# Performance work log

Hardware: AMD Instinct MI355X
Metric: run time of the kernel (lower is better)

## Reference

```python
import jax, jax.numpy as jnp
import numpy as np

B, N_LR, N_HR, D, NH, L, K = 16, 256, 512, 512, 8, 4, 4
FF = 4 * D

def _ln(x, g, b):
    m = jnp.mean(x, -1, keepdims=True)
    v = jnp.var(x, -1, keepdims=True)
    return (x - m) * jax.lax.rsqrt(v + 1e-5) * g + b

def _gelu(x):
    return jax.nn.gelu(x, approximate=False)  # torch nn.GELU default = exact

def _attn(x, qkvW, qkvb, projW, projb, bias):
    b, n, d = x.shape
    hd = d // NH
    qkv = (x @ qkvW + qkvb).reshape(b, n, 3, NH, hd).transpose(2, 0, 3, 1, 4)
    q, k, v = qkv[0], qkv[1], qkv[2]
    a = jnp.einsum('bhnd,bhmd->bhnm', q, k) * (hd ** -0.5)
    if bias is not None:
        a = a + bias
    a = jax.nn.softmax(a, axis=-1)
    o = jnp.einsum('bhnm,bhmd->bhnd', a, v).transpose(0, 2, 1, 3).reshape(b, n, d)
    return o @ projW + projb

def _ffn(x, W1, b1, W2, b2):
    return _gelu(x @ W1 + b1) @ W2 + b2

def setup_inputs() -> dict:
    key = jax.random.key(0)
    ks = iter(jax.random.split(key, 64))
    def rn(shape, s=0.02):
        return jax.random.normal(next(ks), shape, jnp.float32) * s
    inp = {}
    A = rn((B, N_LR, N_LR), 1.0)
    A = 0.5 * (A + A.transpose(0, 2, 1))  # symmetric weighted adjacency
    inp['A_lr'] = A
    inp['X_lr'] = A  # node features = adjacency rows, as in the original model
    inp['ip_W'] = rn((N_LR, D)); inp['ip_b'] = jnp.zeros(D)
    inp['ip_g'] = jnp.ones(D); inp['ip_bt'] = jnp.zeros(D)
    inp['e_n1g'] = jnp.ones((L, D)); inp['e_n1b'] = jnp.zeros((L, D))
    inp['e_qkvW'] = rn((L, D, 3 * D)); inp['e_qkvb'] = jnp.zeros((L, 3 * D))
    inp['e_projW'] = rn((L, D, D)); inp['e_projb'] = jnp.zeros((L, D))
    inp['e_ebW'] = rn((L, NH), 1.0); inp['e_ebs'] = jnp.full((L,), 0.1)
    inp['e_n2g'] = jnp.ones((L, D)); inp['e_n2b'] = jnp.zeros((L, D))
    inp['e_f1W'] = rn((L, D, FF)); inp['e_f1b'] = jnp.zeros((L, FF))
    inp['e_f2W'] = rn((L, FF, D)); inp['e_f2b'] = jnp.zeros((L, D))
    inp['encn_g'] = jnp.ones(D); inp['encn_b'] = jnp.zeros(D)
    inp['up1W'] = rn((N_LR, N_HR)); inp['up1b'] = jnp.zeros(N_HR)
    inp['up2W'] = rn((N_HR, N_HR)); inp['up2b'] = jnp.zeros(N_HR)
    inp['r_n1g'] = jnp.ones(D); inp['r_n1b'] = jnp.zeros(D)
    inp['r_qkvW'] = rn((D, 3 * D)); inp['r_qkvb'] = jnp.zeros(3 * D)
    inp['r_projW'] = rn((D, D)); inp['r_projb'] = jnp.zeros(D)
    inp['r_n2g'] = jnp.ones(D); inp['r_n2b'] = jnp.zeros(D)
    inp['r_f1W'] = rn((D, FF)); inp['r_f1b'] = jnp.zeros(FF)
    inp['r_f2W'] = rn((FF, D)); inp['r_f2b'] = jnp.zeros(D)
    inp['hrn_g'] = jnp.ones(D); inp['hrn_b'] = jnp.zeros(D)
    inp['dec_W'] = rn((K, D, D)); inp['dec_b'] = jnp.full((1,), 3.0)
    return inp

def reference(A_lr, X_lr, ip_W, ip_b, ip_g, ip_bt, e_n1g, e_n1b, e_qkvW, e_qkvb, e_projW, e_projb, e_ebW, e_ebs, e_n2g, e_n2b, e_f1W, e_f1b, e_f2W, e_f2b, encn_g, encn_b, up1W, up1b, up2W, up2b, r_n1g, r_n1b, r_qkvW, r_qkvb, r_projW, r_projb, r_n2g, r_n2b, r_f1W, r_f1b, r_f2W, r_f2b, hrn_g, hrn_b, dec_W, dec_b):
    # input_proj: Linear -> LayerNorm -> GELU (dropout is identity in eval)
    H = _gelu(_ln(X_lr @ ip_W + ip_b, ip_g, ip_bt))  # (B, n_lr, D)
    # encoder: pre-norm blocks with additive per-head edge bias in softmax
    for l in range(L):
        bias = e_ebs[l] * A_lr[:, None, :, :] * e_ebW[l][None, :, None, None]  # (B,NH,N,N)
        H = H + _attn(_ln(H, e_n1g[l], e_n1b[l]), e_qkvW[l], e_qkvb[l], e_projW[l], e_projb[l], bias)
        H = H + _ffn(_ln(H, e_n2g[l], e_n2b[l]), e_f1W[l], e_f1b[l], e_f2W[l], e_f2b[l])
    H = _ln(H, encn_g, encn_b)
    # upsample n_lr -> n_hr along node axis (applied on transposed H)
    Ht = H.transpose(0, 2, 1)                      # (B, D, n_lr)
    Ht = _gelu(Ht @ up1W + up1b) @ up2W + up2b     # (B, D, n_hr)
    H = Ht.transpose(0, 2, 1)                      # (B, n_hr, D)
    # HR refinement: standard pre-norm self-attention block
    H = H + _attn(_ln(H, r_n1g, r_n1b), r_qkvW, r_qkvb, r_projW, r_projb, None)
    H = H + _ffn(_ln(H, r_n2g, r_n2b), r_f1W, r_f1b, r_f2W, r_f2b)
    H = _ln(H, hrn_g, hrn_b)
    # bilinear multi-head decoder: mean_k H W_k H^T, symmetrized
    A_pred = jnp.einsum('bnd,kde,bme->bnm', H, dec_W, H) / K
    A_pred = 0.5 * (A_pred + A_pred.transpose(0, 2, 1))
    iu, ju = np.triu_indices(N_HR, k=1)
    pred = A_pred[:, iu, ju]                        # (B, n_hr*(n_hr-1)/2)
    return jax.nn.softplus(pred + dec_b[0])
```

## Files before the change

kernel.cpp:

```cpp
#include <hip/hip_runtime.h>
#include <hip/hip_bf16.h>
#include <math.h>

#define DEV __device__ __forceinline__

typedef __attribute__((ext_vector_type(8))) short bf16x8;
typedef __attribute__((ext_vector_type(4))) short s16x4;
typedef __attribute__((ext_vector_type(4))) float f32x4;

DEV float gelu_f(float x) {
  float u = 1.5957691f * x * (1.0f + 0.044715f * x * x);
  return x / (1.0f + __expf(-u));
}

DEV short bf16s(float x) {
  __hip_bfloat16 v = __float2bfloat16(x);
  return *reinterpret_cast<short*>(&v);
}

DEV void async16(void* lds, const void* g) {
  __builtin_amdgcn_global_load_lds(
      (const __attribute__((address_space(1))) unsigned int*)g,
      (__attribute__((address_space(3))) unsigned int*)lds, 16, 0, 0);
}

__global__ __launch_bounds__(256) void conv2_kernel(
    const float* __restrict__ X1, __hip_bfloat16* __restrict__ Y1,
    const float* __restrict__ X2, __hip_bfloat16* __restrict__ Y2, int n) {
  int i = blockIdx.x * 256 + threadIdx.x;
  if (i < n) {
    Y1[i] = __float2bfloat16(X1[i]);
    Y2[i] = __float2bfloat16(X2[i]);
  }
}

struct CvArgs {
  const float* s[11];
  __hip_bfloat16* d[11];
};

__global__ __launch_bounds__(256) void multi_tconv_kernel(CvArgs a) {
  const int Rj[11] = {256, 512, 512, 512, 2048, 256, 512, 512, 512, 512, 2048};
  const int Cj[11] = {512, 1536, 512, 2048, 512, 512, 512, 1536, 512, 2048, 512};
  const int Nj[11] = {1, 4, 4, 4, 4, 1, 1, 1, 1, 1, 1};
  __shared__ float t[32][33];
  int rem = blockIdx.x, j = 0;
  for (; j < 11; ++j) {
    int tj = (Rj[j] >> 5) * (Cj[j] >> 5) * Nj[j];
    if (rem < tj) break;
    rem -= tj;
  }
  const int R = Rj[j], C = Cj[j];
  const int perb = (R >> 5) * (C >> 5);
  const int z = rem / perb;
  const int tt = rem % perb;
  const int tc = C >> 5;
  const int r0 = (tt / tc) << 5, c0 = (tt % tc) << 5;
  const float* xb = a.s[j] + (size_t)z * R * C;
  __hip_bfloat16* yb = a.d[j] + (size_t)z * R * C;
  int tx = threadIdx.x & 31, ty = threadIdx.x >> 5;
  for (int i = ty; i < 32; i += 8) t[i][tx] = xb[(size_t)(r0 + i) * C + c0 + tx];
  __syncthreads();
  for (int i = ty; i < 32; i += 8)
    yb[(size_t)(c0 + i) * R + r0 + tx] = __float2bfloat16(t[tx][i]);
}

__global__ __launch_bounds__(256) void build_s_kernel(
    const float* __restrict__ W, __hip_bfloat16* __restrict__ S, int D, int Kk) {
  int i = blockIdx.x * 256 + threadIdx.x;
  if (i >= D * D) return;
  int d = i / D, e = i % D;
  float s = 0.f;
  for (int k = 0; k < Kk; ++k) {
    s += W[(size_t)k * D * D + i];
    s += W[(size_t)k * D * D + (size_t)e * D + d];
  }
  S[i] = __float2bfloat16(s / (2.0f * Kk));
}

template <int NJ>
__global__ __launch_bounds__(256) void mgemm_kernel(
    const __hip_bfloat16* __restrict__ A, const __hip_bfloat16* __restrict__ Bt,
    const float* __restrict__ bias, const float* __restrict__ resid,
    float* __restrict__ outf, __hip_bfloat16* __restrict__ outb,
    int M, int N, int K, int act, int mgrp) {
  __shared__ __align__(16) short As[2][128 * 64];
  __shared__ __align__(16) short Bs[2][NJ * 32 * 64];
  const int tid = threadIdx.x;
  const int lane = tid & 63, wave = tid >> 6;
  const int quad = lane >> 4, l15 = lane & 15;
  const int wr = wave >> 1, wc = wave & 1;
  const int bid = blockIdx.x;
  const int g = bid & 7, sidx = bid >> 3;
  const int mt = g * mgrp + sidx % mgrp;
  const int nt = sidx / mgrp;
  const int row0 = mt * 128, col0 = nt * (NJ * 32);
  const short* Ag = (const short*)A;
  const short* Bg = (const short*)Bt;

  auto stage = [&](int bsel, int k0) {
#pragma unroll
    for (int i = 0; i < 4; ++i) {
      int c = i * 256 + tid;
      int r = c >> 3, pp = c & 7;
      int kc = pp ^ (r & 7);
      async16(&As[bsel][c * 8], &Ag[(size_t)(row0 + r) * K + k0 + kc * 8]);
    }
#pragma unroll
    for (int i = 0; i < NJ; ++i) {
      int c = i * 256 + tid;
      int r = c >> 3, pp = c & 7;
      int kc = pp ^ (r & 7);
      async16(&Bs[bsel][c * 8], &Bg[(size_t)(col0 + r) * K + k0 + kc * 8]);
    }
  };

  f32x4 acc[4][NJ] = {};
  const int nk = K >> 6;
  stage(0, 0);
  for (int t = 0; t < nk; ++t) {
    const int cur = t & 1;
    __syncthreads();
    if (t + 1 < nk) stage(cur ^ 1, (t + 1) << 6);
#pragma unroll
    for (int kh = 0; kh < 2; ++kh) {
      const int ch = ((quad + kh * 4) ^ (l15 & 7)) * 8;
      bf16x8 af[4], bq[NJ];
#pragma unroll
      for (int mi = 0; mi < 4; ++mi)
        af[mi] = *(const bf16x8*)&As[cur][(wr * 64 + mi * 16 + l15) * 64 + ch];
#pragma unroll
      for (int ni = 0; ni < NJ; ++ni)
        bq[ni] = *(const bf16x8*)&Bs[cur][(wc * (NJ * 16) + ni * 16 + l15) * 64 + ch];
#pragma unroll
      for (int mi = 0; mi < 4; ++mi)
#pragma unroll
        for (int ni = 0; ni < NJ; ++ni)
          acc[mi][ni] = __builtin_amdgcn_mfma_f32_16x16x32_bf16(af[mi], bq[ni], acc[mi][ni], 0, 0, 0);
    }
  }

#pragma unroll
  for (int ni = 0; ni < NJ; ++ni) {
    int cc = col0 + wc * (NJ * 16) + ni * 16 + l15;
    float bb = bias ? bias[cc] : 0.f;
#pragma unroll
    for (int mi = 0; mi < 4; ++mi) {
#pragma unroll
      for (int r = 0; r < 4; ++r) {
        int rr = row0 + wr * 64 + mi * 16 + quad * 4 + r;
        size_t idx = (size_t)rr * N + cc;
        float v = acc[mi][ni][r] + bb;
        if (act) v = gelu_f(v);
        if (resid) v += resid[idx];
        if (outf) outf[idx] = v;
        if (outb) outb[idx] = __float2bfloat16(v);
      }
    }
  }
}

__global__ __launch_bounds__(256) void qkv_gemm_kernel(
    const __hip_bfloat16* __restrict__ A, const __hip_bfloat16* __restrict__ Bt,
    const float* __restrict__ bias, __hip_bfloat16* __restrict__ qkv,
    int M, int K, int nseq, int lgn, int mgrp) {
  __shared__ __align__(16) short As[2][128 * 64];
  __shared__ __align__(16) short Bs[2][128 * 64];
  const int tid = threadIdx.x;
  const int lane = tid & 63, wave = tid >> 6;
  const int quad = lane >> 4, l15 = lane & 15;
  const int wr = wave >> 1, wc = wave & 1;
  const int bid = blockIdx.x;
  const int g = bid & 7, sidx = bid >> 3;
  const int mt = g * mgrp + sidx % mgrp;
  const int nt = sidx / mgrp;
  const int row0 = mt * 128, col0 = nt * 128;
  const short* Ag = (const short*)A;
  const short* Bg = (const short*)Bt;

  auto stage = [&](int bsel, int k0) {
#pragma unroll
    for (int i = 0; i < 4; ++i) {
      int c = i * 256 + tid;
      int r = c >> 3, pp = c & 7;
      int kc = pp ^ (r & 7);
      async16(&As[bsel][c * 8], &Ag[(size_t)(row0 + r) * K + k0 + kc * 8]);
    }
#pragma unroll
    for (int i = 0; i < 4; ++i) {
      int c = i * 256 + tid;
      int r = c >> 3, pp = c & 7;
      int kc = pp ^ (r & 7);
      async16(&Bs[bsel][c * 8], &Bg[(size_t)(col0 + r) * K + k0 + kc * 8]);
    }
  };

  f32x4 acc[4][4] = {};
  const int nk = K >> 6;
  stage(0, 0);
  for (int t = 0; t < nk; ++t) {
    const int cur = t & 1;
    __syncthreads();
    if (t + 1 < nk) stage(cur ^ 1, (t + 1) << 6);
#pragma unroll
    for (int kh = 0; kh < 2; ++kh) {
      const int ch = ((quad + kh * 4) ^ (l15 & 7)) * 8;
      bf16x8 af[4], bq[4];
#pragma unroll
      for (int mi = 0; mi < 4; ++mi)
        af[mi] = *(const bf16x8*)&As[cur][(wr * 64 + mi * 16 + l15) * 64 + ch];
#pragma unroll
      for (int ni = 0; ni < 4; ++ni)
        bq[ni] = *(const bf16x8*)&Bs[cur][(wc * 64 + ni * 16 + l15) * 64 + ch];
#pragma unroll
      for (int mi = 0; mi < 4; ++mi)
#pragma unroll
        for (int ni = 0; ni < 4; ++ni)
          acc[mi][ni] = __builtin_amdgcn_mfma_f32_16x16x32_bf16(af[mi], bq[ni], acc[mi][ni], 0, 0, 0);
    }
  }

  const size_t PART = (size_t)M * 512;
#pragma unroll
  for (int ni = 0; ni < 4; ++ni) {
    int cc = col0 + wc * 64 + ni * 16 + l15;
    float bb = bias ? bias[cc] : 0.f;
    int which = cc >> 9;
    int h = (cc >> 6) & 7;
    int d = cc & 63;
#pragma unroll
    for (int mi = 0; mi < 4; ++mi) {
#pragma unroll
      for (int r = 0; r < 4; ++r) {
        int rr = row0 + wr * 64 + mi * 16 + quad * 4 + r;
        int b = rr >> lgn;
        int nn = rr & (nseq - 1);
        float v = acc[mi][ni][r] + bb;
        size_t dst;
        if (which == 2) {
          dst = 2 * PART + (((size_t)b * 8 + h) * 64 + d) * nseq + nn;
        } else {
          dst = (size_t)which * PART + (((size_t)b * 8 + h) * nseq + nn) * 64 + d;
        }
        qkv[dst] = __float2bfloat16(v);
      }
    }
  }
}

__global__ __launch_bounds__(256) void fattn_kernel(
    const __hip_bfloat16* __restrict__ Qh, const __hip_bfloat16* __restrict__ Kh,
    const __hip_bfloat16* __restrict__ Vt, __hip_bfloat16* __restrict__ O,
    const __hip_bfloat16* __restrict__ Abias, const float* __restrict__ ebW,
    const float* __restrict__ ebs, int N, int lgq) {
  __shared__ __align__(16) short Ks[2][64 * 64];
  __shared__ __align__(16) short Vs[2][64 * 64];
  __shared__ __align__(16) short Ps[4][16][72];
  const int bid = blockIdx.x;
  const int g = bid & 7, s = bid >> 3;
  const int bloc = s >> (lgq + 3);
  const int rem = s & ((8 << lgq) - 1);
  const int h = rem >> lgq;
  const int qt = rem & ((1 << lgq) - 1);
  const int b = g * 2 + bloc;
  const int tid = threadIdx.x, lane = tid & 63, wave = tid >> 6;
  const int quad = lane >> 4, l15 = lane & 15;
  const size_t hb = (size_t)b * 8 + h;
  const short* Qg = (const short*)Qh + hb * N * 64;
  const short* Kg = (const short*)Kh + hb * N * 64;
  const short* Vg = (const short*)Vt + hb * 64 * N;
  const float scale = 0.125f;
  const bool hasb = (Abias != nullptr);
  const float bscale = hasb ? ebs[0] * ebW[h] : 0.f;
  const int qrow_w = qt * 64 + wave * 16;

  auto stageKV = [&](int bsel, int k0) {
#pragma unroll
    for (int i = 0; i < 2; ++i) {
      int c = (wave * 2 + i) * 64 + lane;
      int r = c >> 3, pp = c & 7;
      int kc = pp ^ (r & 7);
      async16(&Ks[bsel][(wave * 2 + i) * 512], &Kg[(size_t)(k0 + r) * 64 + kc * 8]);
      async16(&Vs[bsel][(wave * 2 + i) * 512], &Vg[(size_t)r * N + k0 + kc * 8]);
    }
  };

  bf16x8 qf[2];
  qf[0] = *(const bf16x8*)&Qg[(size_t)(qrow_w + l15) * 64 + quad * 8];
  qf[1] = *(const bf16x8*)&Qg[(size_t)(qrow_w + l15) * 64 + quad * 8 + 32];

  float l_r[4] = {0.f, 0.f, 0.f, 0.f};
  f32x4 oacc[4] = {};

  const int ntl = N >> 6;
  stageKV(0, 0);
  for (int t = 0; t < ntl; ++t) {
    const int cur = t & 1;
    const int k0 = t << 6;
    __syncthreads();
    if (t + 1 < ntl) stageKV(cur ^ 1, (t + 1) << 6);

    f32x4 sv[4] = {};
#pragma unroll
    for (int kh = 0; kh < 2; ++kh) {
      const int ch = ((quad + kh * 4) ^ (l15 & 7)) * 8;
#pragma unroll
      for (int ni = 0; ni < 4; ++ni) {
        bf16x8 kf = *(const bf16x8*)&Ks[cur][(ni * 16 + l15) * 64 + ch];
        sv[ni] = __builtin_amdgcn_mfma_f32_16x16x32_bf16(qf[kh], kf, sv[ni], 0, 0, 0);
      }
    }
    if (hasb) {
#pragma unroll
      for (int ni = 0; ni < 4; ++ni)
#pragma unroll
        for (int r = 0; r < 4; ++r) {
          int qq = qrow_w + quad * 4 + r;
          int kk = k0 + ni * 16 + l15;
          float ab = __bfloat162float(Abias[((size_t)b * N + qq) * N + kk]);
          sv[ni][r] = sv[ni][r] * scale + bscale * ab;
        }
    } else {
#pragma unroll
      for (int ni = 0; ni < 4; ++ni)
#pragma unroll
        for (int r = 0; r < 4; ++r) sv[ni][r] *= scale;
    }

#pragma unroll
    for (int ni = 0; ni < 4; ++ni)
#pragma unroll
      for (int r = 0; r < 4; ++r) {
        float p = __expf(sv[ni][r]);
        sv[ni][r] = p;
        l_r[r] += p;
      }

#pragma unroll
    for (int ni = 0; ni < 4; ++ni)
#pragma unroll
      for (int r = 0; r < 4; ++r)
        Ps[wave][quad * 4 + r][ni * 16 + l15] = bf16s(sv[ni][r]);

    bf16x8 pf0 = *(const bf16x8*)&Ps[wave][l15][quad * 8];
    bf16x8 pf1 = *(const bf16x8*)&Ps[wave][l15][quad * 8 + 32];
#pragma unroll
    for (int kh = 0; kh < 2; ++kh) {
      const int ch = ((quad + kh * 4) ^ (l15 & 7)) * 8;
#pragma unroll
      for (int ni = 0; ni < 4; ++ni) {
        bf16x8 vf = *(const bf16x8*)&Vs[cur][(ni * 16 + l15) * 64 + ch];
        oacc[ni] = __builtin_amdgcn_mfma_f32_16x16x32_bf16(kh ? pf1 : pf0, vf, oacc[ni], 0, 0, 0);
      }
    }
  }

#pragma unroll
  for (int off = 1; off < 16; off <<= 1)
#pragma unroll
    for (int r = 0; r < 4; ++r) l_r[r] += __shfl_xor(l_r[r], off, 64);
  float inv[4];
#pragma unroll
  for (int r = 0; r < 4; ++r) inv[r] = 1.f / l_r[r];
#pragma unroll
  for (int ni = 0; ni < 4; ++ni)
#pragma unroll
    for (int r = 0; r < 4; ++r) {
      int nn = qrow_w + quad * 4 + r;
      int col = h * 64 + ni * 16 + l15;
      O[((size_t)b * N + nn) * 512 + col] = __float2bfloat16(oacc[ni][r] * inv[r]);
    }
}

__global__ __launch_bounds__(256) void dec_mfma_kernel(
    const __hip_bfloat16* __restrict__ Tb_, const __hip_bfloat16* __restrict__ Hb_,
    const float* __restrict__ dec_b, float* __restrict__ out) {
  const int Nn = 512, K = 512;
  __shared__ __align__(16) short As[2][64 * 64];
  __shared__ __align__(16) short Bs[2][64 * 64];
  int p = blockIdx.x;
  int bb = blockIdx.y;
  int it = 0, rem = p;
  while (rem >= 8 - it) { rem -= 8 - it; ++it; }
  int jt = it + rem;
  const int row0 = it * 64, col0 = jt * 64;
  const int tid = threadIdx.x;
  const int lane = tid & 63, wave = tid >> 6;
  const int quad = lane >> 4, l15 = lane & 15;
  const int wr = (wave >> 1) * 32, wc = (wave & 1) * 32;
  const short* Ag = (const short*)(Tb_ + (size_t)bb * Nn * K);
  const short* Bg = (const short*)(Hb_ + (size_t)bb * Nn * K);

  auto stage = [&](int bsel, int k0) {
#pragma unroll
    for (int i = 0; i < 2; ++i) {
      int c = (wave * 2 + i) * 64 + lane;
      int r = c >> 3, pp = c & 7;
      int kc = pp ^ (r & 7);
      async16(&As[bsel][(wave * 2 + i) * 512], &Ag[(size_t)(row0 + r) * K + k0 + kc * 8]);
      async16(&Bs[bsel][(wave * 2 + i) * 512], &Bg[(size_t)(col0 + r) * K + k0 + kc * 8]);
    }
  };

  f32x4 acc[2][2] = {};
  const int nk = K >> 6;
  stage(0, 0);
  for (int t = 0; t < nk; ++t) {
    const int cur = t & 1;
    __syncthreads();
    if (t + 1 < nk) stage(cur ^ 1, (t + 1) << 6);
#pragma unroll
    for (int kh = 0; kh < 2; ++kh) {
      const int ch = ((quad + kh * 4) ^ (l15 & 7)) * 8;
      bf16x8 af[2], bq[2];
#pragma unroll
      for (int mi = 0; mi < 2; ++mi)
        af[mi] = *(const bf16x8*)&As[cur][(wr + mi * 16 + l15) * 64 + ch];
#pragma unroll
      for (int ni = 0; ni < 2; ++ni)
        bq[ni] = *(const bf16x8*)&Bs[cur][(wc + ni * 16 + l15) * 64 + ch];
#pragma unroll
      for (int mi = 0; mi < 2; ++mi)
#pragma unroll
        for (int ni = 0; ni < 2; ++ni)
          acc[mi][ni] = __builtin_amdgcn_mfma_f32_16x16x32_bf16(af[mi], bq[ni], acc[mi][ni], 0, 0, 0);
    }
  }

  float db = dec_b[0];
  size_t obase = (size_t)bb * ((size_t)Nn * (Nn - 1) / 2);
#pragma unroll
  for (int mi = 0; mi < 2; ++mi) {
#pragma unroll
    for (int ni = 0; ni < 2; ++ni) {
      int j = col0 + wc + ni * 16 + l15;
#pragma unroll
      for (int r = 0; r < 4; ++r) {
        int i = row0 + wr + mi * 16 + quad * 4 + r;
        if (j > i) {
          float x = acc[mi][ni][r] + db;
          float sp = fmaxf(x, 0.f) + __logf(1.f + __expf(-fabsf(x)));
          out[obase + (size_t)i * (2 * Nn - i - 1) / 2 + (j - i - 1)] = sp;
        }
      }
    }
  }
}

__global__ __launch_bounds__(256) void ln_kernel(
    const float* __restrict__ X, float* __restrict__ outf,
    __hip_bfloat16* __restrict__ outb, const float* __restrict__ g,
    const float* __restrict__ b, int do_gelu) {
  const int row = blockIdx.x * 4 + (threadIdx.x >> 6);
  const int lane = threadIdx.x & 63;
  const float4* x = (const float4*)X + (size_t)row * 128;
  float4 v0 = x[lane], v1 = x[lane + 64];
  float s = v0.x + v0.y + v0.z + v0.w + v1.x + v1.y + v1.z + v1.w;
  float s2 = v0.x * v0.x + v0.y * v0.y + v0.z * v0.z + v0.w * v0.w +
             v1.x * v1.x + v1.y * v1.y + v1.z * v1.z + v1.w * v1.w;
#pragma unroll
  for (int off = 32; off; off >>= 1) {
    s += __shfl_xor(s, off, 64);
    s2 += __shfl_xor(s2, off, 64);
  }
  const float mean = s * (1.0f / 512.0f);
  const float inv = rsqrtf(s2 * (1.0f / 512.0f) - mean * mean + 1e-5f);
  const float4 g0 = ((const float4*)g)[lane], g1 = ((const float4*)g)[lane + 64];
  const float4 b0 = ((const float4*)b)[lane], b1 = ((const float4*)b)[lane + 64];
  float4 y0, y1;
  y0.x = (v0.x - mean) * inv * g0.x + b0.x;
  y0.y = (v0.y - mean) * inv * g0.y + b0.y;
  y0.z = (v0.z - mean) * inv * g0.z + b0.z;
  y0.w = (v0.w - mean) * inv * g0.w + b0.w;
  y1.x = (v1.x - mean) * inv * g1.x + b1.x;
  y1.y = (v1.y - mean) * inv * g1.y + b1.y;
  y1.z = (v1.z - mean) * inv * g1.z + b1.z;
  y1.w = (v1.w - mean) * inv * g1.w + b1.w;
  if (do_gelu) {
    y0.x = gelu_f(y0.x); y0.y = gelu_f(y0.y); y0.z = gelu_f(y0.z); y0.w = gelu_f(y0.w);
    y1.x = gelu_f(y1.x); y1.y = gelu_f(y1.y); y1.z = gelu_f(y1.z); y1.w = gelu_f(y1.w);
  }
  if (outf) {
    float4* of = (float4*)outf + (size_t)row * 128;
    of[lane] = y0;
    of[lane + 64] = y1;
  }
  if (outb) {
    s16x4 p0, p1;
    p0.x = bf16s(y0.x); p0.y = bf16s(y0.y); p0.z = bf16s(y0.z); p0.w = bf16s(y0.w);
    p1.x = bf16s(y1.x); p1.y = bf16s(y1.y); p1.z = bf16s(y1.z); p1.w = bf16s(y1.w);
    *(s16x4*)((short*)outb + (size_t)row * 512 + lane * 4) = p0;
    *(s16x4*)((short*)outb + (size_t)row * 512 + 256 + lane * 4) = p1;
  }
}

template <typename T>
__global__ __launch_bounds__(256) void transpose_kernel(
    const T* __restrict__ X, T* __restrict__ Y, int R, int C) {
  __shared__ T t[32][33];
  const T* xb = X + (size_t)blockIdx.z * R * C;
  T* yb = Y + (size_t)blockIdx.z * R * C;
  int c0 = blockIdx.x * 32, r0 = blockIdx.y * 32;
  int tx = threadIdx.x & 31, ty = threadIdx.x >> 5;
  for (int i = ty; i < 32; i += 8) t[i][tx] = xb[(size_t)(r0 + i) * C + c0 + tx];
  __syncthreads();
  for (int i = ty; i < 32; i += 8) yb[(size_t)(c0 + i) * R + r0 + tx] = t[tx][i];
}

extern "C" void kernel_launch(void* const* d_in, const int* in_sizes, int n_in,
                              void* d_out, int out_size, void* d_ws, size_t ws_size,
                              hipStream_t stream) {
  const float *A_lr = (const float*)d_in[0], *X_lr = (const float*)d_in[1],
              *ip_W = (const float*)d_in[2], *ip_b = (const float*)d_in[3],
              *ip_g = (const float*)d_in[4], *ip_bt = (const float*)d_in[5],
              *e_n1g = (const float*)d_in[6], *e_n1b = (const float*)d_in[7],
              *e_qkvW = (const float*)d_in[8], *e_qkvb = (const float*)d_in[9],
              *e_projW = (const float*)d_in[10], *e_projb = (const float*)d_in[11],
              *e_ebW = (const float*)d_in[12], *e_ebs = (const float*)d_in[13],
              *e_n2g = (const float*)d_in[14], *e_n2b = (const float*)d_in[15],
              *e_f1W = (const float*)d_in[16], *e_f1b = (const float*)d_in[17],
              *e_f2W = (const float*)d_in[18], *e_f2b = (const float*)d_in[19],
              *encn_g = (const float*)d_in[20], *encn_b = (const float*)d_in[21],
              *up1W = (const float*)d_in[22], *up1b = (const float*)d_in[23],
              *up2W = (const float*)d_in[24], *up2b = (const float*)d_in[25],
              *r_n1g = (const float*)d_in[26], *r_n1b = (const float*)d_in[27],
              *r_qkvW = (const float*)d_in[28], *r_qkvb = (const float*)d_in[29],
              *r_projW = (const float*)d_in[30], *r_projb = (const float*)d_in[31],
              *r_n2g = (const float*)d_in[32], *r_n2b = (const float*)d_in[33],
              *r_f1W = (const float*)d_in[34], *r_f1b = (const float*)d_in[35],
              *r_f2W = (const float*)d_in[36], *r_f2b = (const float*)d_in[37],
              *hrn_g = (const float*)d_in[38], *hrn_b = (const float*)d_in[39],
              *dec_W = (const float*)d_in[40], *dec_b = (const float*)d_in[41];

  const int Bb = 16, NLR = 256, NHR = 512, Dm = 512, NHh = 8, FF = 2048, Ll = 4;
  typedef __hip_bfloat16 bf;

  float* ws = (float*)d_ws;
  float* H = ws;
  float* Hf = ws + 4194304;
  bf* XNb = (bf*)(ws + 8388608);
  bf* AOb = (bf*)(ws + 10485760);
  bf* BIGb = (bf*)(ws + 12582912);
  bf* WB = (bf*)(ws + 20971520);
  bf* Xlrb = (bf*)(ws + 29229056);
  bf* Albrb = (bf*)(ws + 29753344);

  size_t o = 0;
  bf* ipWt = WB + o;   o += (size_t)512 * 256;
  bf* eqkvT = WB + o;  o += (size_t)4 * 1536 * 512;
  bf* eprojT = WB + o; o += (size_t)4 * 512 * 512;
  bf* ef1T = WB + o;   o += (size_t)4 * 2048 * 512;
  bf* ef2T = WB + o;   o += (size_t)4 * 512 * 2048;
  bf* up1T = WB + o;   o += (size_t)512 * 256;
  bf* up2T = WB + o;   o += (size_t)512 * 512;
  bf* rqkvT = WB + o;  o += (size_t)1536 * 512;
  bf* rprojT = WB + o; o += (size_t)512 * 512;
  bf* rf1T = WB + o;   o += (size_t)2048 * 512;
  bf* rf2T = WB + o;   o += (size_t)512 * 2048;
  bf* Sb = WB + o;     o += (size_t)512 * 512;

  bf* Q_e = BIGb;
  bf* K_e = BIGb + 2097152;
  bf* V_e = BIGb + 4194304;
  bf* Q_r = BIGb;
  bf* K_r = BIGb + 4194304;
  bf* V_r = BIGb + 8388608;

  CvArgs cv;
  cv.s[0] = ip_W;   cv.d[0] = ipWt;
  cv.s[1] = e_qkvW; cv.d[1] = eqkvT;
  cv.s[2] = e_projW; cv.d[2] = eprojT;
  cv.s[3] = e_f1W;  cv.d[3] = ef1T;
  cv.s[4] = e_f2W;  cv.d[4] = ef2T;
  cv.s[5] = up1W;   cv.d[5] = up1T;
  cv.s[6] = up2W;   cv.d[6] = up2T;
  cv.s[7] = r_qkvW; cv.d[7] = rqkvT;
  cv.s[8] = r_projW; cv.d[8] = rprojT;
  cv.s[9] = r_f1W;  cv.d[9] = rf1T;
  cv.s[10] = r_f2W; cv.d[10] = rf2T;
  multi_tconv_kernel<<<15872, 256, 0, stream>>>(cv);
  conv2_kernel<<<(1048576 + 255) / 256, 256, 0, stream>>>(
      X_lr, Xlrb, A_lr, Albrb, 1048576);
  build_s_kernel<<<(512 * 512 + 255) / 256, 256, 0, stream>>>(dec_W, Sb, Dm, 4);

  mgemm_kernel<2><<<256, 256, 0, stream>>>(
      Xlrb, ipWt, ip_b, nullptr, Hf, nullptr, Bb * NLR, Dm, NLR, 0, 4);
  ln_kernel<<<Bb * NLR / 4, 256, 0, stream>>>(Hf, H, nullptr, ip_g, ip_bt, 1);

  for (int l = 0; l < Ll; ++l) {
    ln_kernel<<<Bb * NLR / 4, 256, 0, stream>>>(H, nullptr, XNb, e_n1g + l * Dm, e_n1b + l * Dm, 0);
    qkv_gemm_kernel<<<384, 256, 0, stream>>>(
        XNb, eqkvT + (size_t)l * 1536 * 512, e_qkvb + l * 1536, BIGb,
        Bb * NLR, Dm, NLR, 8, 4);
    fattn_kernel<<<16 * 8 * 4, 256, 0, stream>>>(
        Q_e, K_e, V_e, AOb, Albrb, e_ebW + l * NHh, e_ebs + l, NLR, 2);
    mgemm_kernel<2><<<256, 256, 0, stream>>>(
        AOb, eprojT + (size_t)l * 512 * 512, e_projb + l * Dm, H,
        H, nullptr, Bb * NLR, Dm, Dm, 0, 4);
    ln_kernel<<<Bb * NLR / 4, 256, 0, stream>>>(H, nullptr, XNb, e_n2g + l * Dm, e_n2b + l * Dm, 0);
    mgemm_kernel<4><<<512, 256, 0, stream>>>(
        XNb, ef1T + (size_t)l * 2048 * 512, e_f1b + l * FF, nullptr,
        nullptr, BIGb, Bb * NLR, FF, Dm, 1, 4);
    mgemm_kernel<2><<<256, 256, 0, stream>>>(
        BIGb, ef2T + (size_t)l * 512 * 2048, e_f2b + l * Dm, H,
        H, nullptr, Bb * NLR, Dm, FF, 0, 4);
  }

  ln_kernel<<<Bb * NLR / 4, 256, 0, stream>>>(H, nullptr, XNb, encn_g, encn_b, 0);
  transpose_kernel<bf><<<dim3(16, 8, Bb), 256, 0, stream>>>(XNb, AOb, NLR, Dm);
  mgemm_kernel<2><<<512, 256, 0, stream>>>(
      AOb, up1T, up1b, nullptr, nullptr, BIGb, Bb * Dm, NHR, NLR, 1, 8);
  mgemm_kernel<2><<<512, 256, 0, stream>>>(
      BIGb, up2T, up2b, nullptr, Hf, nullptr, Bb * Dm, NHR, NHR, 0, 8);
  transpose_kernel<float><<<dim3(16, 16, Bb), 256, 0, stream>>>(Hf, H, Dm, NHR);

  ln_kernel<<<Bb * NHR / 4, 256, 0, stream>>>(H, nullptr, XNb, r_n1g, r_n1b, 0);
  qkv_gemm_kernel<<<768, 256, 0, stream>>>(
      XNb, rqkvT, r_qkvb, BIGb, Bb * NHR, Dm, NHR, 9, 8);
  fattn_kernel<<<16 * 8 * 8, 256, 0, stream>>>(
      Q_r, K_r, V_r, AOb, nullptr, nullptr, nullptr, NHR, 3);
  mgemm_kernel<2><<<512, 256, 0, stream>>>(
      AOb, rprojT, r_projb, H, H, nullptr, Bb * NHR, Dm, Dm, 0, 8);
  ln_kernel<<<Bb * NHR / 4, 256, 0, stream>>>(H, nullptr, XNb, r_n2g, r_n2b, 0);
  mgemm_kernel<4><<<1024, 256, 0, stream>>>(
      XNb, rf1T, r_f1b, nullptr, nullptr, BIGb, Bb * NHR, FF, Dm, 1, 8);
  mgemm_kernel<2><<<512, 256, 0, stream>>>(
      BIGb, rf2T, r_f2b, H, H, nullptr, Bb * NHR, Dm, FF, 0, 8);

  ln_kernel<<<Bb * NHR / 4, 256, 0, stream>>>(H, nullptr, XNb, hrn_g, hrn_b, 0);
  mgemm_kernel<2><<<512, 256, 0, stream>>>(
      XNb, Sb, nullptr, nullptr, nullptr, AOb, Bb * NHR, Dm, Dm, 0, 8);
  dec_mfma_kernel<<<dim3(36, Bb), 256, 0, stream>>>(
      AOb, XNb, dec_b, (float*)d_out);
}
```

Before: 884.5 us.

## Triple-buffer GEMM LDS staging with vmcnt waits and raise MFMA wave priority

Both GEMM kernels move from double to triple-buffered LDS staging. Two k-tiles are prefetched ahead, and explicit s_waitcnt vmcnt counts plus a raw s_barrier replace __syncthreads, so one outstanding tile's loads can stay in flight during compute. MFMA sections in the GEMMs and the attention kernel are wrapped in s_setprio(1)/0 so waves issuing matrix ops get scheduling priority. This raises LDS use by half, which may lower occupancy (about 96KB per block for the qkv kernel). It also depends on the hand-computed vmcnt values matching the number of async loads.

```diff
diff --git a/kernel.cpp b/kernel.cpp
--- a/kernel.cpp
+++ b/kernel.cpp
@@ -84,8 +84,8 @@
     const float* __restrict__ bias, const float* __restrict__ resid,
     float* __restrict__ outf, __hip_bfloat16* __restrict__ outb,
     int M, int N, int K, int act, int mgrp) {
-  __shared__ __align__(16) short As[2][128 * 64];
-  __shared__ __align__(16) short Bs[2][NJ * 32 * 64];
+  __shared__ __align__(16) short As[3][128 * 64];
+  __shared__ __align__(16) short Bs[3][NJ * 32 * 64];
   const int tid = threadIdx.x;
   const int lane = tid & 63, wave = tid >> 6;
   const int quad = lane >> 4, l15 = lane & 15;
@@ -98,30 +98,41 @@
   const short* Ag = (const short*)A;
   const short* Bg = (const short*)Bt;
 
-  auto stage = [&](int bsel, int k0) {
+  auto stage = [&](int buf, int k0) {
 #pragma unroll
     for (int i = 0; i < 4; ++i) {
       int c = i * 256 + tid;
       int r = c >> 3, pp = c & 7;
       int kc = pp ^ (r & 7);
-      async16(&As[bsel][c * 8], &Ag[(size_t)(row0 + r) * K + k0 + kc * 8]);
+      async16(&As[buf][c * 8], &Ag[(size_t)(row0 + r) * K + k0 + kc * 8]);
     }
 #pragma unroll
     for (int i = 0; i < NJ; ++i) {
       int c = i * 256 + tid;
       int r = c >> 3, pp = c & 7;
       int kc = pp ^ (r & 7);
-      async16(&Bs[bsel][c * 8], &Bg[(size_t)(col0 + r) * K + k0 + kc * 8]);
+      async16(&Bs[buf][c * 8], &Bg[(size_t)(col0 + r) * K + k0 + kc * 8]);
     }
   };
 
   f32x4 acc[4][NJ] = {};
   const int nk = K >> 6;
   stage(0, 0);
+  stage(1, 64);
   for (int t = 0; t < nk; ++t) {
-    const int cur = t & 1;
-    __syncthreads();
-    if (t + 1 < nk) stage(cur ^ 1, (t + 1) << 6);
+    int cur = t;
+    while (cur >= 3) cur -= 3;
+    if (t + 1 < nk)
+      asm volatile("s_waitcnt vmcnt(%0)" ::"i"(4 + NJ) : "memory");
+    else
+      asm volatile("s_waitcnt vmcnt(0)" ::: "memory");
+    __builtin_amdgcn_s_barrier();
+    if (t + 2 < nk) {
+      int nb = t + 2;
+      while (nb >= 3) nb -= 3;
+      stage(nb, (t + 2) << 6);
+    }
+    __builtin_amdgcn_s_setprio(1);
 #pragma unroll
     for (int kh = 0; kh < 2; ++kh) {
       const int ch = ((quad + kh * 4) ^ (l15 & 7)) * 8;
@@ -138,6 +149,7 @@
         for (int ni = 0; ni < NJ; ++ni)
           acc[mi][ni] = __builtin_amdgcn_mfma_f32_16x16x32_bf16(af[mi], bq[ni], acc[mi][ni], 0, 0, 0);
     }
+    __builtin_amdgcn_s_setprio(0);
   }
 
 #pragma unroll
@@ -164,8 +176,8 @@
     const __hip_bfloat16* __restrict__ A, const __hip_bfloat16* __restrict__ Bt,
     const float* __restrict__ bias, __hip_bfloat16* __restrict__ qkv,
     int M, int K, int nseq, int lgn, int mgrp) {
-  __shared__ __align__(16) short As[2][128 * 64];
-  __shared__ __align__(16) short Bs[2][128 * 64];
+  __shared__ __align__(16) short As[3][128 * 64];
+  __shared__ __align__(16) short Bs[3][128 * 64];
   const int tid = threadIdx.x;
   const int lane = tid & 63, wave = tid >> 6;
   const int quad = lane >> 4, l15 = lane & 15;
@@ -178,30 +190,41 @@
   const short* Ag = (const short*)A;
   const short* Bg = (const short*)Bt;
 
-  auto stage = [&](int bsel, int k0) {
+  auto stage = [&](int buf, int k0) {
 #pragma unroll
     for (int i = 0; i < 4; ++i) {
       int c = i * 256 + tid;
       int r = c >> 3, pp = c & 7;
       int kc = pp ^ (r & 7);
-      async16(&As[bsel][c * 8], &Ag[(size_t)(row0 + r) * K + k0 + kc * 8]);
+      async16(&As[buf][c * 8], &Ag[(size_t)(row0 + r) * K + k0 + kc * 8]);
     }
 #pragma unroll
     for (int i = 0; i < 4; ++i) {
       int c = i * 256 + tid;
       int r = c >> 3, pp = c & 7;
       int kc = pp ^ (r & 7);
-      async16(&Bs[bsel][c * 8], &Bg[(size_t)(col0 + r) * K + k0 + kc * 8]);
+      async16(&Bs[buf][c * 8], &Bg[(size_t)(col0 + r) * K + k0 + kc * 8]);
     }
   };
 
   f32x4 acc[4][4] = {};
   const int nk = K >> 6;
   stage(0, 0);
+  stage(1, 64);
   for (int t = 0; t < nk; ++t) {
-    const int cur = t & 1;
-    __syncthreads();
-    if (t + 1 < nk) stage(cur ^ 1, (t + 1) << 6);
+    int cur = t;
+    while (cur >= 3) cur -= 3;
+    if (t + 1 < nk)
+      asm volatile("s_waitcnt vmcnt(8)" ::: "memory");
+    else
+      asm volatile("s_waitcnt vmcnt(0)" ::: "memory");
+    __builtin_amdgcn_s_barrier();
+    if (t + 2 < nk) {
+      int nb = t + 2;
+      while (nb >= 3) nb -= 3;
+      stage(nb, (t + 2) << 6);
+    }
+    __builtin_amdgcn_s_setprio(1);
 #pragma unroll
     for (int kh = 0; kh < 2; ++kh) {
       const int ch = ((quad + kh * 4) ^ (l15 & 7)) * 8;
@@ -218,6 +241,7 @@
         for (int ni = 0; ni < 4; ++ni)
           acc[mi][ni] = __builtin_amdgcn_mfma_f32_16x16x32_bf16(af[mi], bq[ni], acc[mi][ni], 0, 0, 0);
     }
+    __builtin_amdgcn_s_setprio(0);
   }
 
   const size_t PART = (size_t)M * 512;
@@ -301,6 +325,7 @@
     if (t + 1 < ntl) stageKV(cur ^ 1, (t + 1) << 6);
 
     f32x4 sv[4] = {};
+    __builtin_amdgcn_s_setprio(1);
 #pragma unroll
     for (int kh = 0; kh < 2; ++kh) {
       const int ch = ((quad + kh * 4) ^ (l15 & 7)) * 8;
@@ -310,6 +335,7 @@
         sv[ni] = __builtin_amdgcn_mfma_f32_16x16x32_bf16(qf[kh], kf, sv[ni], 0, 0, 0);
       }
     }
+    __builtin_amdgcn_s_setprio(0);
     if (hasb) {
 #pragma unroll
       for (int ni = 0; ni < 4; ++ni)
@@ -344,6 +370,7 @@
 
     bf16x8 pf0 = *(const bf16x8*)&Ps[wave][l15][quad * 8];
     bf16x8 pf1 = *(const bf16x8*)&Ps[wave][l15][quad * 8 + 32];
+    __builtin_amdgcn_s_setprio(1);
 #pragma unroll
     for (int kh = 0; kh < 2; ++kh) {
       const int ch = ((quad + kh * 4) ^ (l15 & 7)) * 8;
@@ -353,6 +380,7 @@
         oacc[ni] = __builtin_amdgcn_mfma_f32_16x16x32_bf16(kh ? pf1 : pf0, vf, oacc[ni], 0, 0, 0);
       }
     }
+    __builtin_amdgcn_s_setprio(0);
   }
 
 #pragma unroll
```

Result: slower. 1.013 ms (+14.5%).

## Shrink GEMM tiles to raise grid size and add MFMA priority hints in attention

Applied to the files above, without the earlier changes.

Adds a new 64x64-tile GEMM kernel for the N=512 projections and narrows the 128-wide tiles to 128x64 in the FFN and QKV GEMMs, doubling the block counts to fill more CUs and cut per-block LDS use. It also wraps the MFMA sections of the flash-attention kernel in s_setprio so waves doing matrix math get scheduling priority. Smaller tiles lower data reuse per block and increase global and LDS traffic per flop.

```diff
diff --git a/kernel.cpp b/kernel.cpp
--- a/kernel.cpp
+++ b/kernel.cpp
@@ -78,14 +78,78 @@
   S[i] = __float2bfloat16(s / (2.0f * Kk));
 }
 
-template <int NJ>
-__global__ __launch_bounds__(256) void mgemm_kernel(
+__global__ __launch_bounds__(256) void mgemm64_kernel(
+    const __hip_bfloat16* __restrict__ A, const __hip_bfloat16* __restrict__ Bt,
+    const float* __restrict__ bias, const float* __restrict__ resid,
+    float* __restrict__ outf, __hip_bfloat16* __restrict__ outb,
+    int M, int N, int K, int act, int mgrp) {
+  __shared__ __align__(16) short As[2][64 * 64];
+  __shared__ __align__(16) short Bs[2][64 * 64];
+  const int tid = threadIdx.x;
+  const int lane = tid & 63, wave = tid >> 6;
+  const int quad = lane >> 4, l15 = lane & 15;
+  const int bid = blockIdx.x;
+  const int g = bid & 7, sidx = bid >> 3;
+  const int mt = g * mgrp + sidx % mgrp;
+  const int nt = sidx / mgrp;
+  const int row0 = mt * 64, col0 = nt * 64;
+  const short* Ag = (const short*)A;
+  const short* Bg = (const short*)Bt;
+
+  auto stage = [&](int bsel, int k0) {
+#pragma unroll
+    for (int i = 0; i < 2; ++i) {
+      int c = (wave * 2 + i) * 64 + lane;
+      int r = c >> 3, pp = c & 7;
+      int kc = pp ^ (r & 7);
+      async16(&As[bsel][(wave * 2 + i) * 512], &Ag[(size_t)(row0 + r) * K + k0 + kc * 8]);
+      async16(&Bs[bsel][(wave * 2 + i) * 512], &Bg[(size_t)(col0 + r) * K + k0 + kc * 8]);
+    }
+  };
+
+  f32x4 acc[4] = {};
+  const int nk = K >> 6;
+  stage(0, 0);
+  for (int t = 0; t < nk; ++t) {
+    const int cur = t & 1;
+    __syncthreads();
+    if (t + 1 < nk) stage(cur ^ 1, (t + 1) << 6);
+#pragma unroll
+    for (int kh = 0; kh < 2; ++kh) {
+      const int ch = ((quad + kh * 4) ^ (l15 & 7)) * 8;
+      bf16x8 af = *(const bf16x8*)&As[cur][(wave * 16 + l15) * 64 + ch];
+#pragma unroll
+      for (int ni = 0; ni < 4; ++ni) {
+        bf16x8 bq = *(const bf16x8*)&Bs[cur][(ni * 16 + l15) * 64 + ch];
+        acc[ni] = __builtin_amdgcn_mfma_f32_16x16x32_bf16(af, bq, acc[ni], 0, 0, 0);
+      }
+    }
+  }
+
+#pragma unroll
+  for (int ni = 0; ni < 4; ++ni) {
+    int cc = col0 + ni * 16 + l15;
+    float bb = bias ? bias[cc] : 0.f;
+#pragma unroll
+    for (int r = 0; r < 4; ++r) {
+      int rr = row0 + wave * 16 + quad * 4 + r;
+      size_t idx = (size_t)rr * N + cc;
+      float v = acc[ni][r] + bb;
+      if (act) v = gelu_f(v);
+      if (resid) v += resid[idx];
+      if (outf) outf[idx] = v;
+      if (outb) outb[idx] = __float2bfloat16(v);
+    }
+  }
+}
+
+__global__ __launch_bounds__(256) void mgemm128_kernel(
     const __hip_bfloat16* __restrict__ A, const __hip_bfloat16* __restrict__ Bt,
     const float* __restrict__ bias, const float* __restrict__ resid,
     float* __restrict__ outf, __hip_bfloat16* __restrict__ outb,
     int M, int N, int K, int act, int mgrp) {
   __shared__ __align__(16) short As[2][128 * 64];
-  __shared__ __align__(16) short Bs[2][NJ * 32 * 64];
+  __shared__ __align__(16) short Bs[2][64 * 64];
   const int tid = threadIdx.x;
   const int lane = tid & 63, wave = tid >> 6;
   const int quad = lane >> 4, l15 = lane & 15;
@@ -94,7 +158,7 @@
   const int g = bid & 7, sidx = bid >> 3;
   const int mt = g * mgrp + sidx % mgrp;
   const int nt = sidx / mgrp;
-  const int row0 = mt * 128, col0 = nt * (NJ * 32);
+  const int row0 = mt * 128, col0 = nt * 64;
   const short* Ag = (const short*)A;
   const short* Bg = (const short*)Bt;
 
@@ -107,7 +171,7 @@
       async16(&As[bsel][c * 8], &Ag[(size_t)(row0 + r) * K + k0 + kc * 8]);
     }
 #pragma unroll
-    for (int i = 0; i < NJ; ++i) {
+    for (int i = 0; i < 2; ++i) {
       int c = i * 256 + tid;
       int r = c >> 3, pp = c & 7;
       int kc = pp ^ (r & 7);
@@ -115,7 +179,7 @@
     }
   };
 
-  f32x4 acc[4][NJ] = {};
+  f32x4 acc[4][2] = {};
   const int nk = K >> 6;
   stage(0, 0);
   for (int t = 0; t < nk; ++t) {
@@ -125,24 +189,24 @@
 #pragma unroll
     for (int kh = 0; kh < 2; ++kh) {
       const int ch = ((quad + kh * 4) ^ (l15 & 7)) * 8;
-      bf16x8 af[4], bq[NJ];
+      bf16x8 af[4], bq[2];
 #pragma unroll
       for (int mi = 0; mi < 4; ++mi)
         af[mi] = *(const bf16x8*)&As[cur][(wr * 64 + mi * 16 + l15) * 64 + ch];
 #pragma unroll
-      for (int ni = 0; ni < NJ; ++ni)
-        bq[ni] = *(const bf16x8*)&Bs[cur][(wc * (NJ * 16) + ni * 16 + l15) * 64 + ch];
+      for (int ni = 0; ni < 2; ++ni)
+        bq[ni] = *(const bf16x8*)&Bs[cur][(wc * 32 + ni * 16 + l15) * 64 + ch];
 #pragma unroll
       for (int mi = 0; mi < 4; ++mi)
 #pragma unroll
-        for (int ni = 0; ni < NJ; ++ni)
+        for (int ni = 0; ni < 2; ++ni)
           acc[mi][ni] = __builtin_amdgcn_mfma_f32_16x16x32_bf16(af[mi], bq[ni], acc[mi][ni], 0, 0, 0);
     }
   }
 
 #pragma unroll
-  for (int ni = 0; ni < NJ; ++ni) {
-    int cc = col0 + wc * (NJ * 16) + ni * 16 + l15;
+  for (int ni = 0; ni < 2; ++ni) {
+    int cc = col0 + wc * 32 + ni * 16 + l15;
     float bb = bias ? bias[cc] : 0.f;
 #pragma unroll
     for (int mi = 0; mi < 4; ++mi) {
@@ -165,7 +229,7 @@
     const float* __restrict__ bias, __hip_bfloat16* __restrict__ qkv,
     int M, int K, int nseq, int lgn, int mgrp) {
   __shared__ __align__(16) short As[2][128 * 64];
-  __shared__ __align__(16) short Bs[2][128 * 64];
+  __shared__ __align__(16) short Bs[2][64 * 64];
   const int tid = threadIdx.x;
   const int lane = tid & 63, wave = tid >> 6;
   const int quad = lane >> 4, l15 = lane & 15;
@@ -174,7 +238,7 @@
   const int g = bid & 7, sidx = bid >> 3;
   const int mt = g * mgrp + sidx % mgrp;
   const int nt = sidx / mgrp;
-  const int row0 = mt * 128, col0 = nt * 128;
+  const int row0 = mt * 128, col0 = nt * 64;
   const short* Ag = (const short*)A;
   const short* Bg = (const short*)Bt;
 
@@ -187,7 +251,7 @@
       async16(&As[bsel][c * 8], &Ag[(size_t)(row0 + r) * K + k0 + kc * 8]);
     }
 #pragma unroll
-    for (int i = 0; i < 4; ++i) {
+    for (int i = 0; i < 2; ++i) {
       int c = i * 256 + tid;
       int r = c >> 3, pp = c & 7;
       int kc = pp ^ (r & 7);
@@ -195,7 +259,7 @@
     }
   };
 
-  f32x4 acc[4][4] = {};
+  f32x4 acc[4][2] = {};
   const int nk = K >> 6;
   stage(0, 0);
   for (int t = 0; t < nk; ++t) {
@@ -205,25 +269,25 @@
 #pragma unroll
     for (int kh = 0; kh < 2; ++kh) {
       const int ch = ((quad + kh * 4) ^ (l15 & 7)) * 8;
-      bf16x8 af[4], bq[4];
+      bf16x8 af[4], bq[2];
 #pragma unroll
       for (int mi = 0; mi < 4; ++mi)
         af[mi] = *(const bf16x8*)&As[cur][(wr * 64 + mi * 16 + l15) * 64 + ch];
 #pragma unroll
-      for (int ni = 0; ni < 4; ++ni)
-        bq[ni] = *(const bf16x8*)&Bs[cur][(wc * 64 + ni * 16 + l15) * 64 + ch];
+      for (int ni = 0; ni < 2; ++ni)
+        bq[ni] = *(const bf16x8*)&Bs[cur][(wc * 32 + ni * 16 + l15) * 64 + ch];
 #pragma unroll
       for (int mi = 0; mi < 4; ++mi)
 #pragma unroll
-        for (int ni = 0; ni < 4; ++ni)
+        for (int ni = 0; ni < 2; ++ni)
           acc[mi][ni] = __builtin_amdgcn_mfma_f32_16x16x32_bf16(af[mi], bq[ni], acc[mi][ni], 0, 0, 0);
     }
   }
 
   const size_t PART = (size_t)M * 512;
 #pragma unroll
-  for (int ni = 0; ni < 4; ++ni) {
-    int cc = col0 + wc * 64 + ni * 16 + l15;
+  for (int ni = 0; ni < 2; ++ni) {
+    int cc = col0 + wc * 32 + ni * 16 + l15;
     float bb = bias ? bias[cc] : 0.f;
     int which = cc >> 9;
     int h = (cc >> 6) & 7;
@@ -301,6 +365,7 @@
     if (t + 1 < ntl) stageKV(cur ^ 1, (t + 1) << 6);
 
     f32x4 sv[4] = {};
+    __builtin_amdgcn_s_setprio(1);
 #pragma unroll
     for (int kh = 0; kh < 2; ++kh) {
       const int ch = ((quad + kh * 4) ^ (l15 & 7)) * 8;
@@ -310,6 +375,7 @@
         sv[ni] = __builtin_amdgcn_mfma_f32_16x16x32_bf16(qf[kh], kf, sv[ni], 0, 0, 0);
       }
     }
+    __builtin_amdgcn_s_setprio(0);
     if (hasb) {
 #pragma unroll
       for (int ni = 0; ni < 4; ++ni)
@@ -344,6 +410,7 @@
 
     bf16x8 pf0 = *(const bf16x8*)&Ps[wave][l15][quad * 8];
     bf16x8 pf1 = *(const bf16x8*)&Ps[wave][l15][quad * 8 + 32];
+    __builtin_amdgcn_s_setprio(1);
 #pragma unroll
     for (int kh = 0; kh < 2; ++kh) {
       const int ch = ((quad + kh * 4) ^ (l15 & 7)) * 8;
@@ -353,6 +420,7 @@
         oacc[ni] = __builtin_amdgcn_mfma_f32_16x16x32_bf16(kh ? pf1 : pf0, vf, oacc[ni], 0, 0, 0);
       }
     }
+    __builtin_amdgcn_s_setprio(0);
   }
 
 #pragma unroll
@@ -583,53 +651,53 @@
       X_lr, Xlrb, A_lr, Albrb, 1048576);
   build_s_kernel<<<(512 * 512 + 255) / 256, 256, 0, stream>>>(dec_W, Sb, Dm, 4);
 
-  mgemm_kernel<2><<<256, 256, 0, stream>>>(
-      Xlrb, ipWt, ip_b, nullptr, Hf, nullptr, Bb * NLR, Dm, NLR, 0, 4);
+  mgemm64_kernel<<<512, 256, 0, stream>>>(
+      Xlrb, ipWt, ip_b, nullptr, Hf, nullptr, Bb * NLR, Dm, NLR, 0, 8);
   ln_kernel<<<Bb * NLR / 4, 256, 0, stream>>>(Hf, H, nullptr, ip_g, ip_bt, 1);
 
   for (int l = 0; l < Ll; ++l) {
     ln_kernel<<<Bb * NLR / 4, 256, 0, stream>>>(H, nullptr, XNb, e_n1g + l * Dm, e_n1b + l * Dm, 0);
-    qkv_gemm_kernel<<<384, 256, 0, stream>>>(
+    qkv_gemm_kernel<<<768, 256, 0, stream>>>(
         XNb, eqkvT + (size_t)l * 1536 * 512, e_qkvb + l * 1536, BIGb,
         Bb * NLR, Dm, NLR, 8, 4);
     fattn_kernel<<<16 * 8 * 4, 256, 0, stream>>>(
         Q_e, K_e, V_e, AOb, Albrb, e_ebW + l * NHh, e_ebs + l, NLR, 2);
-    mgemm_kernel<2><<<256, 256, 0, stream>>>(
+    mgemm64_kernel<<<512, 256, 0, stream>>>(
         AOb, eprojT + (size_t)l * 512 * 512, e_projb + l * Dm, H,
-        H, nullptr, Bb * NLR, Dm, Dm, 0, 4);
+        H, nullptr, Bb * NLR, Dm, Dm, 0, 8);
     ln_kernel<<<Bb * NLR / 4, 256, 0, stream>>>(H, nullptr, XNb, e_n2g + l * Dm, e_n2b + l * Dm, 0);
-    mgemm_kernel<4><<<512, 256, 0, stream>>>(
+    mgemm128_kernel<<<1024, 256, 0, stream>>>(
         XNb, ef1T + (size_t)l * 2048 * 512, e_f1b + l * FF, nullptr,
         nullptr, BIGb, Bb * NLR, FF, Dm, 1, 4);
-    mgemm_kernel<2><<<256, 256, 0, stream>>>(
+    mgemm64_kernel<<<512, 256, 0, stream>>>(
         BIGb, ef2T + (size_t)l * 512 * 2048, e_f2b + l * Dm, H,
-        H, nullptr, Bb * NLR, Dm, FF, 0, 4);
+        H, nullptr, Bb * NLR, Dm, FF, 0, 8);
   }
 
   ln_kernel<<<Bb * NLR / 4, 256, 0, stream>>>(H, nullptr, XNb, encn_g, encn_b, 0);
   transpose_kernel<bf><<<dim3(16, 8, Bb), 256, 0, stream>>>(XNb, AOb, NLR, Dm);
-  mgemm_kernel<2><<<512, 256, 0, stream>>>(
-      AOb, up1T, up1b, nullptr, nullptr, BIGb, Bb * Dm, NHR, NLR, 1, 8);
-  mgemm_kernel<2><<<512, 256, 0, stream>>>(
-      BIGb, up2T, up2b, nullptr, Hf, nullptr, Bb * Dm, NHR, NHR, 0, 8);
+  mgemm64_kernel<<<1024, 256, 0, stream>>>(
+      AOb, up1T, up1b, nullptr, nullptr, BIGb, Bb * Dm, NHR, NLR, 1, 16);
+  mgemm64_kernel<<<1024, 256, 0, stream>>>(
+      BIGb, up2T, up2b, nullptr, Hf, nullptr, Bb * Dm, NHR, NHR, 0, 16);
   transpose_kernel<float><<<dim3(16, 16, Bb), 256, 0, stream>>>(Hf, H, Dm, NHR);
 
   ln_kernel<<<Bb * NHR / 4, 256, 0, stream>>>(H, nullptr, XNb, r_n1g, r_n1b, 0);
-  qkv_gemm_kernel<<<768, 256, 0, stream>>>(
+  qkv_gemm_kernel<<<1536, 256, 0, stream>>>(
       XNb, rqkvT, r_qkvb, BIGb, Bb * NHR, Dm, NHR, 9, 8);
   fattn_kernel<<<16 * 8 * 8, 256, 0, stream>>>(
       Q_r, K_r, V_r, AOb, nullptr, nullptr, nullptr, NHR, 3);
-  mgemm_kernel<2><<<512, 256, 0, stream>>>(
-      AOb, rprojT, r_projb, H, H, nullptr, Bb * NHR, Dm, Dm, 0, 8);
+  mgemm64_kernel<<<1024, 256, 0, stream>>>(
+      AOb, rprojT, r_projb, H, H, nullptr, Bb * NHR, Dm, Dm, 0, 16);
   ln_kernel<<<Bb * NHR / 4, 256, 0, stream>>>(H, nullptr, XNb, r_n2g, r_n2b, 0);
-  mgemm_kernel<4><<<1024, 256, 0, stream>>>(
+  mgemm128_kernel<<<2048, 256, 0, stream>>>(
       XNb, rf1T, r_f1b, nullptr, nullptr, BIGb, Bb * NHR, FF, Dm, 1, 8);
-  mgemm_kernel<2><<<512, 256, 0, stream>>>(
-      BIGb, rf2T, r_f2b, H, H, nullptr, Bb * NHR, Dm, FF, 0, 8);
+  mgemm64_kernel<<<1024, 256, 0, stream>>>(
+      BIGb, rf2T, r_f2b, H, H, nullptr, Bb * NHR, Dm, FF, 0, 16);
 
   ln_kernel<<<Bb * NHR / 4, 256, 0, stream>>>(H, nullptr, XNb, hrn_g, hrn_b, 0);
-  mgemm_kernel<2><<<512, 256, 0, stream>>>(
-      XNb, Sb, nullptr, nullptr, nullptr, AOb, Bb * NHR, Dm, Dm, 0, 8);
+  mgemm64_kernel<<<1024, 256, 0, stream>>>(
+      XNb, Sb, nullptr, nullptr, nullptr, AOb, Bb * NHR, Dm, Dm, 0, 16);
   dec_mfma_kernel<<<dim3(36, Bb), 256, 0, stream>>>(
       AOb, XNb, dec_b, (float*)d_out);
 }
```

Result: faster. 812.9 us (-8.1%).
